# Kernel tuning notes

Hardware: AMD Instinct MI355X
Metric: run time of the kernel (lower is better)

## Reference

```python
import jax, jax.numpy as jnp
import numpy as np

B, T, HID = 2, 2048, 1024
H, DK, DV = 8, 128, 128      # num_heads, head_f_dim (key), head_i_dim (value)
LR = 128                     # gate low-rank dim
EPS = 1e-5


def setup_inputs() -> dict:
    key = jax.random.key(0)
    ks = jax.random.split(key, 8)
    def w(k, shape, fan_in):
        return jax.random.normal(k, shape, jnp.float32) / np.float32(np.sqrt(fan_in))
    return {
        "hidden_states": jax.random.normal(ks[0], (B, T, HID), jnp.float32),
        "Wq": w(ks[1], (HID, HID), HID),   # key_dim x hidden
        "Wk": w(ks[2], (HID, HID), HID),
        "Wv": w(ks[3], (HID, HID), HID),   # value_dim x hidden
        "Wg1": w(ks[4], (LR, HID), HID),   # low-rank gate down
        "Wg2": w(ks[5], (HID, LR), LR),    # low-rank gate up
        "g_norm_weight": jnp.ones((HID,), jnp.float32),
        "Wo": w(ks[6], (HID, HID), HID),
    }


def _lightnet_fwd(x, Wq, Wk, Wv, Wg1, Wg2, g_norm_weight, Wo):
    b, t, _ = x.shape
    q = jax.nn.silu(x @ Wq.T).reshape(b, t, H, DK)
    k = (x @ Wk.T).reshape(b, t, H, DK)
    v = (x @ Wv.T).reshape(b, t, H, DV)

    # LightNet gating: normalized keys via logcumsumexp over time
    z = jax.lax.cumlogsumexp(k, axis=1)                 # [b,t,h,dk]
    k = jnp.exp(k - z)                                  # exp-normalized keys
    g = jnp.concatenate([z[:, :1], z[:, :-1]], axis=1) - z  # <= 0; g[:,0]=0

    scale = DK ** -0.5

    # gated linear attention recurrence: S_t = exp(g_t) * S_{t-1} + k_t v_t^T
    def step(S, inp):
        qt, kt, vt, gt = inp                            # [b,h,dk],[b,h,dk],[b,h,dv],[b,h,dk]
        S = jnp.exp(gt)[..., None] * S + kt[..., None] * vt[..., None, :]
        o = jnp.einsum('bhk,bhkv->bhv', qt, S) * scale
        return S, o

    S0 = jnp.zeros((b, H, DK, DV), x.dtype)
    tfirst = lambda a: jnp.moveaxis(a, 1, 0)
    _, oT = jax.lax.scan(step, S0, (tfirst(q), tfirst(k), tfirst(v), tfirst(g)))
    o = jnp.moveaxis(oT, 0, 1).reshape(b, t, H * DV)    # [b,t,hidden]

    # RMSNorm(o) * swish(gate) then output projection
    gate = (x @ Wg1.T) @ Wg2.T
    o = o * jax.lax.rsqrt(jnp.mean(o * o, axis=-1, keepdims=True) + EPS) * g_norm_weight
    o = o * gate * jax.nn.sigmoid(gate)
    return o @ Wo.T


def reference(hidden_states, Wq, Wk, Wv, Wg1, Wg2, g_norm_weight, Wo):
    return _lightnet_fwd(hidden_states, Wq, Wk, Wv, Wg1, Wg2, g_norm_weight, Wo)
```

## Files before the change

kernel.cpp:

```cpp
#include <hip/hip_runtime.h>
#include <hip/hip_bf16.h>
#include <stdint.h>


typedef short short8 __attribute__((ext_vector_type(8)));
typedef float f32x4 __attribute__((ext_vector_type(4)));

#define T_SEQ 2048
#define HIDN  1024
#define SCALE 0.08838834764831845f
#define LDSP  136

__device__ __forceinline__ float blo(unsigned int u){
  union{unsigned int i; float f;} v; v.i = u << 16; return v.f;
}
__device__ __forceinline__ float bhi(unsigned int u){
  union{unsigned int i; float f;} v; v.i = u & 0xffff0000u; return v.f;
}
__device__ __forceinline__ float bu2f(unsigned short u){
  union{unsigned int i; float f;} v; v.i = ((unsigned int)u) << 16; return v.f;
}
__device__ __forceinline__ unsigned short f2bu(float f){
  union{float f; unsigned int i;} v; v.f = f;
  unsigned int x = v.i;
  x += 0x7fffu + ((x >> 16) & 1u);
  return (unsigned short)(x >> 16);
}
__device__ __forceinline__ void up8(const unsigned short* p, float* f){
  uint4 v = *(const uint4*)p;
  f[0]=blo(v.x); f[1]=bhi(v.x); f[2]=blo(v.y); f[3]=bhi(v.y);
  f[4]=blo(v.z); f[5]=bhi(v.z); f[6]=blo(v.w); f[7]=bhi(v.w);
}
__device__ __forceinline__ void async16(const void* g, void* l){
  __builtin_amdgcn_global_load_lds(
      (const __attribute__((address_space(1))) unsigned int*)g,
      (__attribute__((address_space(3))) unsigned int*)l, 16, 0, 0);
}

__global__ __launch_bounds__(256) void convert_all(
    const float* __restrict__ X,  const float* __restrict__ Wq,
    const float* __restrict__ Wk, const float* __restrict__ Wv,
    const float* __restrict__ Wg1,const float* __restrict__ Wg2,
    const float* __restrict__ gnw,const float* __restrict__ Wo,
    unsigned short* __restrict__ base, float* __restrict__ SumSq)
{
  int q = blockIdx.x * 256 + threadIdx.x;
  const float* src; unsigned short* dst; int rel = q;
  if (rel < 1048576)            { src = X;   dst = base;            }
  else if ((rel -= 1048576) < 262144) { src = Wq;  dst = base + 4194304; }
  else if ((rel -=  262144) < 262144) { src = Wk;  dst = base + 5242880; }
  else if ((rel -=  262144) < 262144) { src = Wv;  dst = base + 6291456; }
  else if ((rel -=  262144) < 262144) { src = Wo;  dst = base + 7340032; }
  else if ((rel -=  262144) <  32768) { src = Wg1; dst = base + 8388608; }
  else if ((rel -=   32768) <  32768) { src = Wg2; dst = base + 8519680; }
  else if ((rel -=   32768) <    256) { src = gnw; dst = base + 8650752; }
  else { rel -= 256;
    ((float4*)SumSq)[rel] = make_float4(0.f,0.f,0.f,0.f); return; }
  float4 v = ((const float4*)src)[rel];
  ushort4 o; o.x=f2bu(v.x); o.y=f2bu(v.y); o.z=f2bu(v.z); o.w=f2bu(v.w);
  ((ushort4*)dst)[rel] = o;
}

__device__ __forceinline__ void gemm_core(
    const unsigned short* __restrict__ A, const unsigned short* __restrict__ B,
    int K, int row0, int col0,
    unsigned short* sA, unsigned short* sB, f32x4 acc[4][4], int tid)
{
  const int lane = tid & 63;
  const int wm = (tid >> 6) & 1, wn = tid >> 7;
  const int wb = tid & 192;
  for (int k0 = 0; k0 < K; k0 += 64){
    __syncthreads();
#pragma unroll
    for (int h = 0; h < 2; ++h){
#pragma unroll
      for (int r = 0; r < 2; ++r){
        int idx  = r*256 + tid;
        int mrow = idx >> 2, kc = (idx & 3) * 8;
        async16(A + (size_t)(row0 + mrow)*K + k0 + h*32 + kc,
                sA + (size_t)(h*512 + r*256 + wb)*8);
        async16(B + (size_t)(col0 + mrow)*K + k0 + h*32 + kc,
                sB + (size_t)(h*512 + r*256 + wb)*8);
      }
    }
    __syncthreads();
#pragma unroll
    for (int h = 0; h < 2; ++h){
      short8 av[4], bv[4];
#pragma unroll
      for (int i=0;i<4;i++)
        av[i] = *(const short8*)(sA + h*4096 + (size_t)(wm*64 + i*16 + (lane&15))*32 + (lane>>4)*8);
#pragma unroll
      for (int j=0;j<4;j++)
        bv[j] = *(const short8*)(sB + h*4096 + (size_t)(wn*64 + j*16 + (lane&15))*32 + (lane>>4)*8);
#pragma unroll
      for (int i=0;i<4;i++)
#pragma unroll
        for (int j=0;j<4;j++)
          acc[i][j] = __builtin_amdgcn_mfma_f32_16x16x32_bf16(av[i], bv[j], acc[i][j], 0, 0, 0);
    }
  }
}

__device__ __forceinline__ void epilogue_lds(
    f32x4 acc[4][4], int row0, int col0, int tid, int ldc, int act,
    unsigned short* __restrict__ Cb, unsigned short* sC)
{
  const int lane = tid & 63;
  const int wm = (tid >> 6) & 1, wn = tid >> 7;
#pragma unroll
  for (int p=0;p<4;p++){
    __syncthreads();
    if (wm == (p>>1)){
#pragma unroll
      for (int ii=0; ii<2; ii++){
        int i = (p&1)*2 + ii;
        int lr = i*16 + ((lane>>4)<<2) - (p&1)*32;
#pragma unroll
        for (int j=0;j<4;j++){
          int col = wn*64 + j*16 + (lane&15);
#pragma unroll
          for (int r=0;r<4;r++){
            float v = acc[i][j][r];
            if (act == 1) v = v / (1.f + __expf(-v));
            else if (act == 2) v = __expf(v);
            sC[(lr+r)*128 + col] = f2bu(v);
          }
        }
      }
    }
    __syncthreads();
#pragma unroll
    for (int c = tid; c < 512; c += 256){
      int rr = c >> 4, off = (c & 15)*8;
      *(uint4*)&Cb[(size_t)(row0 + p*32 + rr)*ldc + col0 + off] =
          *(const uint4*)&sC[rr*128 + off];
    }
  }
}

__device__ __forceinline__ void epilogue_f32(
    f32x4 acc[4][4], int row0, int col0, int tid, int ldc,
    float* __restrict__ Cf)
{
  const int lane = tid & 63;
  const int wm = (tid >> 6) & 1, wn = tid >> 7;
#pragma unroll
  for (int i=0;i<4;i++){
    int rbase = row0 + wm*64 + i*16 + ((lane>>4)<<2);
#pragma unroll
    for (int j=0;j<4;j++){
      int col = col0 + wn*64 + j*16 + (lane&15);
#pragma unroll
      for (int r=0;r<4;r++)
        Cf[(size_t)(rbase + r)*ldc + col] = acc[i][j][r];
    }
  }
}

__global__ __launch_bounds__(256, 4) void proj_kernel(
    const unsigned short* __restrict__ X,
    const unsigned short* __restrict__ Wq, const unsigned short* __restrict__ Wk,
    const unsigned short* __restrict__ Wv, const unsigned short* __restrict__ Wg1,
    unsigned short* __restrict__ Qb, unsigned short* __restrict__ Eb,
    unsigned short* __restrict__ Vb, unsigned short* __restrict__ G1b)
{
  __shared__ unsigned short sA[128*64], sB[128*64];
  int tid = threadIdx.x;
  int which = blockIdx.y >> 3;
  const unsigned short* Bp = (which==0)?Wq:(which==1)?Wk:(which==2)?Wv:Wg1;
  int row0 = blockIdx.x * 128;
  int col0 = (which==3) ? 0 : (blockIdx.y & 7) * 128;
  f32x4 acc[4][4] = {};
  gemm_core(X, Bp, HIDN, row0, col0, sA, sB, acc, tid);
  if      (which==0) epilogue_lds(acc,row0,col0,tid,HIDN,1,Qb, sA);
  else if (which==1) epilogue_lds(acc,row0,col0,tid,HIDN,2,Eb, sA);
  else if (which==2) epilogue_lds(acc,row0,col0,tid,HIDN,0,Vb, sA);
  else               epilogue_lds(acc,row0,col0,tid,128 ,0,G1b,sA);
}

__global__ __launch_bounds__(256, 4) void gemm_bt(
    const unsigned short* __restrict__ A, const unsigned short* __restrict__ B,
    int K, int ldc, int act, float* __restrict__ Cf,
    unsigned short* __restrict__ Cb)
{
  __shared__ unsigned short sA[128*64], sB[128*64];
  int tid = threadIdx.x;
  int row0 = blockIdx.x * 128, col0 = blockIdx.y * 128;
  f32x4 acc[4][4] = {};
  gemm_core(A, B, K, row0, col0, sA, sB, acc, tid);
  if (Cb) epilogue_lds(acc, row0, col0, tid, ldc, act, Cb, sA);
  else    epilogue_f32(acc, row0, col0, tid, ldc, Cf);
}

__global__ __launch_bounds__(512, 2) void attn_pass1(
    const unsigned short* __restrict__ Eb, const unsigned short* __restrict__ Vb,
    unsigned short* __restrict__ U, float* __restrict__ Esum)
{
  __shared__ unsigned short Vt[128*LDSP], Et[128*LDSP];
  __shared__ float seg_part[4*128];
  int tid = threadIdx.x;
  const int lane = tid & 63, quad = lane >> 4;
  const int w = tid >> 6, wm = w & 3, wn = w >> 2;
  const int Rb = wm*32, Cb = wn*64;
  int bh = blockIdx.x >> 4, ch = blockIdx.x & 15;
  int b = bh >> 3, h = bh & 7;
  size_t rowbase = (size_t)(b*T_SEQ + ch*128)*HIDN + h*128;

#pragma unroll
  for (int i=0;i<4;i++){
    int u = tid + i*512; int t = u >> 4, kc = (u & 15)*8;
    unsigned short tmp[8];
    *(uint4*)tmp = *(const uint4*)&Vb[rowbase + (size_t)t*HIDN + kc];
#pragma unroll
    for (int j=0;j<8;j++) Vt[(kc+j)*LDSP + t] = tmp[j];
    *(uint4*)tmp = *(const uint4*)&Eb[rowbase + (size_t)t*HIDN + kc];
#pragma unroll
    for (int j=0;j<8;j++) Et[(kc+j)*LDSP + t] = tmp[j];
  }
  __syncthreads();

  {
    int seg = tid >> 7, k = tid & 127;
    float s = 0.f;
    for (int c = seg*32; c < seg*32+32; ++c) s += bu2f(Et[k*LDSP + c]);
    seg_part[seg*128 + k] = s;
  }
  __syncthreads();
  if (tid < 128)
    Esum[(size_t)blockIdx.x*128 + tid] =
        seg_part[tid] + seg_part[128+tid] + seg_part[256+tid] + seg_part[384+tid];

  f32x4 acc[2][4] = {};
  short8 av[2], bv[4];
#pragma unroll
  for (int s0=0; s0<128; s0+=32){
#pragma unroll
    for (int i=0;i<2;i++)
      av[i] = *(const short8*)(Vt + (Rb + i*16 + (lane&15))*LDSP + s0 + quad*8);
#pragma unroll
    for (int j=0;j<4;j++)
      bv[j] = *(const short8*)(Et + (Cb + j*16 + (lane&15))*LDSP + s0 + quad*8);
#pragma unroll
    for (int i=0;i<2;i++)
#pragma unroll
      for (int j=0;j<4;j++)
        acc[i][j] = __builtin_amdgcn_mfma_f32_16x16x32_bf16(av[i], bv[j], acc[i][j], 0,0,0);
  }
  __syncthreads();

#pragma unroll
  for (int i=0;i<2;i++)
#pragma unroll
    for (int j=0;j<4;j++){
      int k = Cb + j*16 + (lane&15);
#pragma unroll
      for (int r=0;r<4;r++){
        int v = Rb + i*16 + quad*4 + r;
        Et[v*LDSP + k] = f2bu(acc[i][j][r]);
      }
    }
  __syncthreads();
  unsigned short* Ub = U + (size_t)blockIdx.x*16384;
#pragma unroll
  for (int i=0;i<4;i++){
    int u = tid + i*512; int v = u >> 4, kc = (u & 15)*8;
    *(uint4*)&Ub[v*128 + kc] = *(const uint4*)&Et[v*LDSP + kc];
  }
}

__global__ __launch_bounds__(256) void attn_pass2(
    unsigned short* __restrict__ U, float* __restrict__ Esum)
{
  int bh = blockIdx.x >> 4, sl = blockIdx.x & 15;
  int p = sl*1024 + threadIdx.x*4;
  float r0=0.f, r1=0.f, r2=0.f, r3=0.f;
  for (int c=0;c<16;c++){
    ushort4* ptr = (ushort4*)&U[(size_t)(bh*16 + c)*16384 + p];
    ushort4 t = *ptr;
    ushort4 w;
    w.x=f2bu(r0); w.y=f2bu(r1); w.z=f2bu(r2); w.w=f2bu(r3);
    *ptr = w;
    r0 += bu2f(t.x); r1 += bu2f(t.y); r2 += bu2f(t.z); r3 += bu2f(t.w);
  }
  if (sl == 0 && threadIdx.x < 128){
    float r = 0.f;
    for (int c=0;c<16;c++){
      float* q = &Esum[(size_t)(bh*16 + c)*128 + threadIdx.x];
      float t = *q; *q = r; r += t;
    }
  }
}

__global__ __launch_bounds__(512, 4) void attn_pass3(
    const unsigned short* __restrict__ Eb, const unsigned short* __restrict__ Qb,
    const unsigned short* __restrict__ Vb, const unsigned short* __restrict__ U,
    const float* __restrict__ Esum, unsigned short* __restrict__ Oatt,
    float* __restrict__ SumSq)
{
  __shared__ unsigned short smem[2*128*LDSP];
  __shared__ float seg_part[4*128];
  unsigned short* bufA = smem;
  unsigned short* bufB = smem + 128*LDSP;

  int tid = threadIdx.x;
  const int lane = tid & 63, quad = lane >> 4;
  const int w = tid >> 6, wm = w & 3, wn = w >> 2;
  const int Rb = wm*32, Cb = wn*64;
  int bh = blockIdx.x >> 4, ch = blockIdx.x & 15;
  int b = bh >> 3, h = bh & 7;
  size_t rowbase = (size_t)(b*T_SEQ + ch*128)*HIDN + h*128;
  const unsigned short* Ublk = U + (size_t)blockIdx.x*16384;

#pragma unroll
  for (int i=0;i<4;i++){
    int u = tid + i*512; int t = u >> 4, kc = (u & 15)*8;
    *(uint4*)&bufA[t*LDSP + kc] = *(const uint4*)&Qb[rowbase + (size_t)t*HIDN + kc];
    *(uint4*)&bufB[t*LDSP + kc] = *(const uint4*)&Eb[rowbase + (size_t)t*HIDN + kc];
  }
  __syncthreads();

  {
    int col = tid & 127, seg = tid >> 7;
    float psum = 0.f;
    for (int s = seg*32; s < seg*32+32; ++s) psum += bu2f(bufB[s*LDSP + col]);
    seg_part[seg*128 + col] = psum;
    __syncthreads();
    float run = Esum[(size_t)blockIdx.x*128 + col];
    for (int ss=0; ss<4; ++ss) if (ss < seg) run += seg_part[ss*128 + col];
    for (int s = seg*32; s < seg*32+32; ++s){
      run += bu2f(bufB[s*LDSP + col]);
      float q = bu2f(bufA[s*LDSP + col]);
      bufA[s*LDSP + col] = f2bu(q * SCALE * __builtin_amdgcn_rcpf(run));
    }
  }
  __syncthreads();

  f32x4 accO[2][4] = {}, accP[2][4] = {};
  short8 av[2], bv[4];
#pragma unroll
  for (int k0=0; k0<128; k0+=32){
#pragma unroll
    for (int i=0;i<2;i++)
      av[i] = *(const short8*)(bufA + (Rb + i*16 + (lane&15))*LDSP + k0 + quad*8);
#pragma unroll
    for (int j=0;j<4;j++)
      bv[j] = *(const short8*)(Ublk + (size_t)(Cb + j*16 + (lane&15))*128 + k0 + quad*8);
#pragma unroll
    for (int i=0;i<2;i++)
#pragma unroll
      for (int j=0;j<4;j++)
        accO[i][j] = __builtin_amdgcn_mfma_f32_16x16x32_bf16(av[i], bv[j], accO[i][j], 0,0,0);
#pragma unroll
    for (int j=0;j<4;j++)
      bv[j] = *(const short8*)(bufB + (Cb + j*16 + (lane&15))*LDSP + k0 + quad*8);
#pragma unroll
    for (int i=0;i<2;i++)
#pragma unroll
      for (int j=0;j<4;j++)
        accP[i][j] = __builtin_amdgcn_mfma_f32_16x16x32_bf16(av[i], bv[j], accP[i][j], 0,0,0);
  }
  __syncthreads();

#pragma unroll
  for (int i=0;i<2;i++){
#pragma unroll
    for (int j=0;j<4;j++){
      int s = Cb + j*16 + (lane&15);
#pragma unroll
      for (int r=0;r<4;r++){
        int t = Rb + i*16 + quad*4 + r;
        bufA[t*LDSP + s] = f2bu(s <= t ? accP[i][j][r] : 0.f);
      }
    }
  }
#pragma unroll
  for (int i=0;i<4;i++){
    int u = tid + i*512; int t = u >> 4, kc = (u & 15)*8;
    unsigned short tmp[8];
    *(uint4*)tmp = *(const uint4*)&Vb[rowbase + (size_t)t*HIDN + kc];
#pragma unroll
    for (int j=0;j<8;j++) bufB[(kc+j)*LDSP + t] = tmp[j];
  }
  __syncthreads();

#pragma unroll
  for (int k0=0; k0<128; k0+=32){
#pragma unroll
    for (int i=0;i<2;i++)
      av[i] = *(const short8*)(bufA + (Rb + i*16 + (lane&15))*LDSP + k0 + quad*8);
#pragma unroll
    for (int j=0;j<4;j++)
      bv[j] = *(const short8*)(bufB + (Cb + j*16 + (lane&15))*LDSP + k0 + quad*8);
#pragma unroll
    for (int i=0;i<2;i++)
#pragma unroll
      for (int j=0;j<4;j++)
        accO[i][j] = __builtin_amdgcn_mfma_f32_16x16x32_bf16(av[i], bv[j], accO[i][j], 0,0,0);
  }
  __syncthreads();

#pragma unroll
  for (int i=0;i<2;i++){
#pragma unroll
    for (int j=0;j<4;j++){
      int v = Cb + j*16 + (lane&15);
#pragma unroll
      for (int r=0;r<4;r++){
        int t = Rb + i*16 + quad*4 + r;
        bufA[t*LDSP + v] = f2bu(accO[i][j][r]);
      }
    }
  }
  __syncthreads();

  {
    int seg = tid >> 7, row = tid & 127;
    float s = 0.f;
    for (int c = seg*32; c < seg*32+32; ++c){
      float x = bu2f(bufA[row*LDSP + c]); s += x*x;
    }
    seg_part[seg*128 + row] = s;
  }
#pragma unroll
  for (int i=0;i<4;i++){
    int u = tid + i*512; int t = u >> 4, kc = (u & 15)*8;
    *(uint4*)&Oatt[rowbase + (size_t)t*HIDN + kc] = *(const uint4*)&bufA[t*LDSP + kc];
  }
  __syncthreads();
  if (tid < 128){
    float s = seg_part[tid] + seg_part[128+tid] + seg_part[256+tid] + seg_part[384+tid];
    atomicAdd(&SumSq[(size_t)b*T_SEQ + ch*128 + tid], s);
  }
}

__global__ __launch_bounds__(256) void norm_gate2(
    const unsigned short* __restrict__ Oatt, const unsigned short* __restrict__ Gt,
    const unsigned short* __restrict__ gnw, const float* __restrict__ SumSq,
    unsigned short* __restrict__ Onorm)
{
  int row = blockIdx.x, tid = threadIdx.x;
  float rstd = rsqrtf(SumSq[row] * (1.f/1024.f) + 1e-5f);
  ushort4 o4 = *(const ushort4*)&Oatt[(size_t)row*HIDN + tid*4];
  ushort4 g4 = *(const ushort4*)&Gt  [(size_t)row*HIDN + tid*4];
  ushort4 w4 = *(const ushort4*)&gnw[tid*4];
  ushort4 r4;
  r4.x = f2bu(bu2f(o4.x) * rstd * bu2f(w4.x) * bu2f(g4.x));
  r4.y = f2bu(bu2f(o4.y) * rstd * bu2f(w4.y) * bu2f(g4.y));
  r4.z = f2bu(bu2f(o4.z) * rstd * bu2f(w4.z) * bu2f(g4.z));
  r4.w = f2bu(bu2f(o4.w) * rstd * bu2f(w4.w) * bu2f(g4.w));
  *(ushort4*)&Onorm[(size_t)row*HIDN + tid*4] = r4;
}

extern "C" void kernel_launch(void* const* d_in, const int* in_sizes, int n_in,
                              void* d_out, int out_size, void* d_ws, size_t ws_size,
                              hipStream_t stream) {
  unsigned short* wsS = (unsigned short*)d_ws;

  unsigned short* Xc   = wsS;
  unsigned short* Wqc  = wsS + 4194304;
  unsigned short* Wkc  = wsS + 5242880;
  unsigned short* Wvc  = wsS + 6291456;
  unsigned short* Woc  = wsS + 7340032;
  unsigned short* Wg1c = wsS + 8388608;
  unsigned short* Wg2c = wsS + 8519680;
  unsigned short* gnwc = wsS + 8650752;
  unsigned short* Qb   = wsS + 8651776;
  unsigned short* Eb   = wsS + 12846080;
  unsigned short* Vb   = wsS + 17040384;
  unsigned short* G1b  = wsS + 21234688;
  unsigned short* Gt   = wsS + 21758976;
  unsigned short* Ub   = wsS + 25953280;
  unsigned short* Oattb= wsS + 30147584;
  float*          Esum = (float*)(wsS + 34341888);
  float*          SumSq= (float*)(wsS + 34407424);
  unsigned short* Onorm = Qb;

  convert_all<<<8453, 256, 0, stream>>>(
      (const float*)d_in[0], (const float*)d_in[1], (const float*)d_in[2],
      (const float*)d_in[3], (const float*)d_in[4], (const float*)d_in[5],
      (const float*)d_in[6], (const float*)d_in[7], wsS, SumSq);

  proj_kernel<<<dim3(32,25), 256, 0, stream>>>(Xc, Wqc, Wkc, Wvc, Wg1c, Qb, Eb, Vb, G1b);
  gemm_bt   <<<dim3(32,8),  256, 0, stream>>>(G1b, Wg2c, 128, HIDN, 1, nullptr, Gt);
  attn_pass1<<<256, 512, 0, stream>>>(Eb, Vb, Ub, Esum);
  attn_pass2<<<256, 256, 0, stream>>>(Ub, Esum);
  attn_pass3<<<256, 512, 0, stream>>>(Eb, Qb, Vb, Ub, Esum, Oattb, SumSq);
  norm_gate2<<<4096, 256, 0, stream>>>(Oattb, Gt, gnwc, SumSq, Onorm);
  gemm_bt   <<<dim3(32,8),  256, 0, stream>>>(Onorm, Woc, HIDN, HIDN, 0,
                                              (float*)d_out, nullptr);
}
```

Measured before the change: 206.2 us.

## Fuse attention passes and norm-gate into one cooperative kernel with grid syncs

Merges the three chunked-attention passes and the RMSNorm/gate kernel into a single cooperative kernel, using grid-wide syncs between the phases. Each block keeps its attention output tile in LDS and applies the norm and gate directly from there. This removes three kernel launches and the intermediate Oatt write and read through global memory. In exchange it pays for three grid barriers and requires all 256 blocks to be co-resident, and launch bounds no longer hint occupancy.

```diff
diff --git a/kernel.cpp b/kernel.cpp
--- a/kernel.cpp
+++ b/kernel.cpp
@@ -1,6 +1,9 @@
 #include <hip/hip_runtime.h>
 #include <hip/hip_bf16.h>
+#include <hip/hip_cooperative_groups.h>
 #include <stdint.h>
+
+namespace cg = cooperative_groups;
 
 
 typedef short short8 __attribute__((ext_vector_type(8)));
@@ -193,17 +196,25 @@
   else    epilogue_f32(acc, row0, col0, tid, ldc, Cf);
 }
 
-__global__ __launch_bounds__(512, 2) void attn_pass1(
-    const unsigned short* __restrict__ Eb, const unsigned short* __restrict__ Vb,
-    unsigned short* __restrict__ U, float* __restrict__ Esum)
-{
-  __shared__ unsigned short Vt[128*LDSP], Et[128*LDSP];
+__global__ __launch_bounds__(512) void attn_fused(
+    const unsigned short* __restrict__ Eb, const unsigned short* __restrict__ Qb,
+    const unsigned short* __restrict__ Vb, unsigned short* __restrict__ U,
+    float* __restrict__ Esum, float* __restrict__ SumSq,
+    const unsigned short* __restrict__ Gt, const unsigned short* __restrict__ gnw,
+    unsigned short* __restrict__ Onorm)
+{
+  cg::grid_group gridg = cg::this_grid();
+  __shared__ unsigned short smem[2*128*LDSP];
   __shared__ float seg_part[4*128];
+  unsigned short* bufA = smem;
+  unsigned short* bufB = smem + 128*LDSP;
+
   int tid = threadIdx.x;
   const int lane = tid & 63, quad = lane >> 4;
   const int w = tid >> 6, wm = w & 3, wn = w >> 2;
-  const int Rb = wm*32, Cb = wn*64;
-  int bh = blockIdx.x >> 4, ch = blockIdx.x & 15;
+  const int Rb = wm*32, Cbnd = wn*64;
+  int blk = blockIdx.x;
+  int bh = blk >> 4, ch = blk & 15;
   int b = bh >> 3, h = bh & 7;
   size_t rowbase = (size_t)(b*T_SEQ + ch*128)*HIDN + h*128;
 
@@ -213,104 +224,88 @@
     unsigned short tmp[8];
     *(uint4*)tmp = *(const uint4*)&Vb[rowbase + (size_t)t*HIDN + kc];
 #pragma unroll
-    for (int j=0;j<8;j++) Vt[(kc+j)*LDSP + t] = tmp[j];
+    for (int j=0;j<8;j++) bufA[(kc+j)*LDSP + t] = tmp[j];
     *(uint4*)tmp = *(const uint4*)&Eb[rowbase + (size_t)t*HIDN + kc];
 #pragma unroll
-    for (int j=0;j<8;j++) Et[(kc+j)*LDSP + t] = tmp[j];
+    for (int j=0;j<8;j++) bufB[(kc+j)*LDSP + t] = tmp[j];
   }
   __syncthreads();
 
   {
     int seg = tid >> 7, k = tid & 127;
     float s = 0.f;
-    for (int c = seg*32; c < seg*32+32; ++c) s += bu2f(Et[k*LDSP + c]);
+    for (int c = seg*32; c < seg*32+32; ++c) s += bu2f(bufB[k*LDSP + c]);
     seg_part[seg*128 + k] = s;
   }
   __syncthreads();
   if (tid < 128)
-    Esum[(size_t)blockIdx.x*128 + tid] =
+    Esum[(size_t)blk*128 + tid] =
         seg_part[tid] + seg_part[128+tid] + seg_part[256+tid] + seg_part[384+tid];
 
-  f32x4 acc[2][4] = {};
-  short8 av[2], bv[4];
-#pragma unroll
-  for (int s0=0; s0<128; s0+=32){
+  {
+    f32x4 acc[2][4] = {};
+    short8 av[2], bv[4];
+#pragma unroll
+    for (int s0=0; s0<128; s0+=32){
+#pragma unroll
+      for (int i=0;i<2;i++)
+        av[i] = *(const short8*)(bufA + (Rb + i*16 + (lane&15))*LDSP + s0 + quad*8);
+#pragma unroll
+      for (int j=0;j<4;j++)
+        bv[j] = *(const short8*)(bufB + (Cbnd + j*16 + (lane&15))*LDSP + s0 + quad*8);
+#pragma unroll
+      for (int i=0;i<2;i++)
+#pragma unroll
+        for (int j=0;j<4;j++)
+          acc[i][j] = __builtin_amdgcn_mfma_f32_16x16x32_bf16(av[i], bv[j], acc[i][j], 0,0,0);
+    }
+    __syncthreads();
 #pragma unroll
     for (int i=0;i<2;i++)
-      av[i] = *(const short8*)(Vt + (Rb + i*16 + (lane&15))*LDSP + s0 + quad*8);
-#pragma unroll
-    for (int j=0;j<4;j++)
-      bv[j] = *(const short8*)(Et + (Cb + j*16 + (lane&15))*LDSP + s0 + quad*8);
-#pragma unroll
-    for (int i=0;i<2;i++)
-#pragma unroll
-      for (int j=0;j<4;j++)
-        acc[i][j] = __builtin_amdgcn_mfma_f32_16x16x32_bf16(av[i], bv[j], acc[i][j], 0,0,0);
-  }
-  __syncthreads();
-
-#pragma unroll
-  for (int i=0;i<2;i++)
-#pragma unroll
-    for (int j=0;j<4;j++){
-      int k = Cb + j*16 + (lane&15);
-#pragma unroll
-      for (int r=0;r<4;r++){
-        int v = Rb + i*16 + quad*4 + r;
-        Et[v*LDSP + k] = f2bu(acc[i][j][r]);
-      }
-    }
-  __syncthreads();
-  unsigned short* Ub = U + (size_t)blockIdx.x*16384;
-#pragma unroll
-  for (int i=0;i<4;i++){
-    int u = tid + i*512; int v = u >> 4, kc = (u & 15)*8;
-    *(uint4*)&Ub[v*128 + kc] = *(const uint4*)&Et[v*LDSP + kc];
-  }
-}
-
-__global__ __launch_bounds__(256) void attn_pass2(
-    unsigned short* __restrict__ U, float* __restrict__ Esum)
-{
-  int bh = blockIdx.x >> 4, sl = blockIdx.x & 15;
-  int p = sl*1024 + threadIdx.x*4;
-  float r0=0.f, r1=0.f, r2=0.f, r3=0.f;
-  for (int c=0;c<16;c++){
-    ushort4* ptr = (ushort4*)&U[(size_t)(bh*16 + c)*16384 + p];
-    ushort4 t = *ptr;
-    ushort4 w;
-    w.x=f2bu(r0); w.y=f2bu(r1); w.z=f2bu(r2); w.w=f2bu(r3);
-    *ptr = w;
-    r0 += bu2f(t.x); r1 += bu2f(t.y); r2 += bu2f(t.z); r3 += bu2f(t.w);
-  }
-  if (sl == 0 && threadIdx.x < 128){
-    float r = 0.f;
-    for (int c=0;c<16;c++){
-      float* q = &Esum[(size_t)(bh*16 + c)*128 + threadIdx.x];
-      float t = *q; *q = r; r += t;
-    }
-  }
-}
-
-__global__ __launch_bounds__(512, 4) void attn_pass3(
-    const unsigned short* __restrict__ Eb, const unsigned short* __restrict__ Qb,
-    const unsigned short* __restrict__ Vb, const unsigned short* __restrict__ U,
-    const float* __restrict__ Esum, unsigned short* __restrict__ Oatt,
-    float* __restrict__ SumSq)
-{
-  __shared__ unsigned short smem[2*128*LDSP];
-  __shared__ float seg_part[4*128];
-  unsigned short* bufA = smem;
-  unsigned short* bufB = smem + 128*LDSP;
-
-  int tid = threadIdx.x;
-  const int lane = tid & 63, quad = lane >> 4;
-  const int w = tid >> 6, wm = w & 3, wn = w >> 2;
-  const int Rb = wm*32, Cb = wn*64;
-  int bh = blockIdx.x >> 4, ch = blockIdx.x & 15;
-  int b = bh >> 3, h = bh & 7;
-  size_t rowbase = (size_t)(b*T_SEQ + ch*128)*HIDN + h*128;
-  const unsigned short* Ublk = U + (size_t)blockIdx.x*16384;
+#pragma unroll
+      for (int j=0;j<4;j++){
+        int k = Cbnd + j*16 + (lane&15);
+#pragma unroll
+        for (int r=0;r<4;r++){
+          int v = Rb + i*16 + quad*4 + r;
+          bufB[v*LDSP + k] = f2bu(acc[i][j][r]);
+        }
+      }
+    __syncthreads();
+    unsigned short* Ub = U + (size_t)blk*16384;
+#pragma unroll
+    for (int i=0;i<4;i++){
+      int u = tid + i*512; int v = u >> 4, kc = (u & 15)*8;
+      *(uint4*)&Ub[v*128 + kc] = *(const uint4*)&bufB[v*LDSP + kc];
+    }
+  }
+  __threadfence();
+  gridg.sync();
+
+  {
+    int sl = blk & 15;
+    if (tid < 256){
+      int p = sl*1024 + tid*4;
+      float r0=0.f, r1=0.f, r2=0.f, r3=0.f;
+      for (int c=0;c<16;c++){
+        ushort4* ptr = (ushort4*)&U[(size_t)(bh*16 + c)*16384 + p];
+        ushort4 t = *ptr;
+        ushort4 wv;
+        wv.x=f2bu(r0); wv.y=f2bu(r1); wv.z=f2bu(r2); wv.w=f2bu(r3);
+        *ptr = wv;
+        r0 += bu2f(t.x); r1 += bu2f(t.y); r2 += bu2f(t.z); r3 += bu2f(t.w);
+      }
+    }
+    if (sl == 0 && tid < 128){
+      float r = 0.f;
+      for (int c=0;c<16;c++){
+        float* q = &Esum[(size_t)(bh*16 + c)*128 + tid];
+        float t = *q; *q = r; r += t;
+      }
+    }
+  }
+  __threadfence();
+  gridg.sync();
 
 #pragma unroll
   for (int i=0;i<4;i++){
@@ -326,7 +321,7 @@
     for (int s = seg*32; s < seg*32+32; ++s) psum += bu2f(bufB[s*LDSP + col]);
     seg_part[seg*128 + col] = psum;
     __syncthreads();
-    float run = Esum[(size_t)blockIdx.x*128 + col];
+    float run = Esum[(size_t)blk*128 + col];
     for (int ss=0; ss<4; ++ss) if (ss < seg) run += seg_part[ss*128 + col];
     for (int s = seg*32; s < seg*32+32; ++s){
       run += bu2f(bufB[s*LDSP + col]);
@@ -337,28 +332,31 @@
   __syncthreads();
 
   f32x4 accO[2][4] = {}, accP[2][4] = {};
-  short8 av[2], bv[4];
-#pragma unroll
-  for (int k0=0; k0<128; k0+=32){
-#pragma unroll
-    for (int i=0;i<2;i++)
-      av[i] = *(const short8*)(bufA + (Rb + i*16 + (lane&15))*LDSP + k0 + quad*8);
-#pragma unroll
-    for (int j=0;j<4;j++)
-      bv[j] = *(const short8*)(Ublk + (size_t)(Cb + j*16 + (lane&15))*128 + k0 + quad*8);
-#pragma unroll
-    for (int i=0;i<2;i++)
+  {
+    const unsigned short* Ublk = U + (size_t)blk*16384;
+    short8 av[2], bv[4];
+#pragma unroll
+    for (int k0=0; k0<128; k0+=32){
+#pragma unroll
+      for (int i=0;i<2;i++)
+        av[i] = *(const short8*)(bufA + (Rb + i*16 + (lane&15))*LDSP + k0 + quad*8);
 #pragma unroll
       for (int j=0;j<4;j++)
-        accO[i][j] = __builtin_amdgcn_mfma_f32_16x16x32_bf16(av[i], bv[j], accO[i][j], 0,0,0);
-#pragma unroll
-    for (int j=0;j<4;j++)
-      bv[j] = *(const short8*)(bufB + (Cb + j*16 + (lane&15))*LDSP + k0 + quad*8);
-#pragma unroll
-    for (int i=0;i<2;i++)
+        bv[j] = *(const short8*)(Ublk + (size_t)(Cbnd + j*16 + (lane&15))*128 + k0 + quad*8);
+#pragma unroll
+      for (int i=0;i<2;i++)
+#pragma unroll
+        for (int j=0;j<4;j++)
+          accO[i][j] = __builtin_amdgcn_mfma_f32_16x16x32_bf16(av[i], bv[j], accO[i][j], 0,0,0);
 #pragma unroll
       for (int j=0;j<4;j++)
-        accP[i][j] = __builtin_amdgcn_mfma_f32_16x16x32_bf16(av[i], bv[j], accP[i][j], 0,0,0);
+        bv[j] = *(const short8*)(bufB + (Cbnd + j*16 + (lane&15))*LDSP + k0 + quad*8);
+#pragma unroll
+      for (int i=0;i<2;i++)
+#pragma unroll
+        for (int j=0;j<4;j++)
+          accP[i][j] = __builtin_amdgcn_mfma_f32_16x16x32_bf16(av[i], bv[j], accP[i][j], 0,0,0);
+    }
   }
   __syncthreads();
 
@@ -366,7 +364,7 @@
   for (int i=0;i<2;i++){
 #pragma unroll
     for (int j=0;j<4;j++){
-      int s = Cb + j*16 + (lane&15);
+      int s = Cbnd + j*16 + (lane&15);
 #pragma unroll
       for (int r=0;r<4;r++){
         int t = Rb + i*16 + quad*4 + r;
@@ -384,19 +382,22 @@
   }
   __syncthreads();
 
-#pragma unroll
-  for (int k0=0; k0<128; k0+=32){
-#pragma unroll
-    for (int i=0;i<2;i++)
-      av[i] = *(const short8*)(bufA + (Rb + i*16 + (lane&15))*LDSP + k0 + quad*8);
-#pragma unroll
-    for (int j=0;j<4;j++)
-      bv[j] = *(const short8*)(bufB + (Cb + j*16 + (lane&15))*LDSP + k0 + quad*8);
-#pragma unroll
-    for (int i=0;i<2;i++)
+  {
+    short8 av[2], bv[4];
+#pragma unroll
+    for (int k0=0; k0<128; k0+=32){
+#pragma unroll
+      for (int i=0;i<2;i++)
+        av[i] = *(const short8*)(bufA + (Rb + i*16 + (lane&15))*LDSP + k0 + quad*8);
 #pragma unroll
       for (int j=0;j<4;j++)
-        accO[i][j] = __builtin_amdgcn_mfma_f32_16x16x32_bf16(av[i], bv[j], accO[i][j], 0,0,0);
+        bv[j] = *(const short8*)(bufB + (Cbnd + j*16 + (lane&15))*LDSP + k0 + quad*8);
+#pragma unroll
+      for (int i=0;i<2;i++)
+#pragma unroll
+        for (int j=0;j<4;j++)
+          accO[i][j] = __builtin_amdgcn_mfma_f32_16x16x32_bf16(av[i], bv[j], accO[i][j], 0,0,0);
+    }
   }
   __syncthreads();
 
@@ -404,7 +405,7 @@
   for (int i=0;i<2;i++){
 #pragma unroll
     for (int j=0;j<4;j++){
-      int v = Cb + j*16 + (lane&15);
+      int v = Cbnd + j*16 + (lane&15);
 #pragma unroll
       for (int r=0;r<4;r++){
         int t = Rb + i*16 + quad*4 + r;
@@ -422,34 +423,27 @@
     }
     seg_part[seg*128 + row] = s;
   }
-#pragma unroll
-  for (int i=0;i<4;i++){
-    int u = tid + i*512; int t = u >> 4, kc = (u & 15)*8;
-    *(uint4*)&Oatt[rowbase + (size_t)t*HIDN + kc] = *(const uint4*)&bufA[t*LDSP + kc];
-  }
   __syncthreads();
   if (tid < 128){
     float s = seg_part[tid] + seg_part[128+tid] + seg_part[256+tid] + seg_part[384+tid];
     atomicAdd(&SumSq[(size_t)b*T_SEQ + ch*128 + tid], s);
   }
-}
-
-__global__ __launch_bounds__(256) void norm_gate2(
-    const unsigned short* __restrict__ Oatt, const unsigned short* __restrict__ Gt,
-    const unsigned short* __restrict__ gnw, const float* __restrict__ SumSq,
-    unsigned short* __restrict__ Onorm)
-{
-  int row = blockIdx.x, tid = threadIdx.x;
-  float rstd = rsqrtf(SumSq[row] * (1.f/1024.f) + 1e-5f);
-  ushort4 o4 = *(const ushort4*)&Oatt[(size_t)row*HIDN + tid*4];
-  ushort4 g4 = *(const ushort4*)&Gt  [(size_t)row*HIDN + tid*4];
-  ushort4 w4 = *(const ushort4*)&gnw[tid*4];
-  ushort4 r4;
-  r4.x = f2bu(bu2f(o4.x) * rstd * bu2f(w4.x) * bu2f(g4.x));
-  r4.y = f2bu(bu2f(o4.y) * rstd * bu2f(w4.y) * bu2f(g4.y));
-  r4.z = f2bu(bu2f(o4.z) * rstd * bu2f(w4.z) * bu2f(g4.z));
-  r4.w = f2bu(bu2f(o4.w) * rstd * bu2f(w4.w) * bu2f(g4.w));
-  *(ushort4*)&Onorm[(size_t)row*HIDN + tid*4] = r4;
+  __threadfence();
+  gridg.sync();
+
+#pragma unroll
+  for (int i=0;i<4;i++){
+    int u = tid + i*512; int t = u >> 4, kc = (u & 15)*8;
+    float rstd = rsqrtf(SumSq[(size_t)b*T_SEQ + ch*128 + t] * (1.f/1024.f) + 1e-5f);
+    float o[8], g[8], wv[8];
+    up8(&bufA[t*LDSP + kc], o);
+    up8(&Gt[rowbase + (size_t)t*HIDN + kc], g);
+    up8(&gnw[h*128 + kc], wv);
+    unsigned short r8[8];
+#pragma unroll
+    for (int j=0;j<8;j++) r8[j] = f2bu(o[j] * rstd * wv[j] * g[j]);
+    *(uint4*)&Onorm[rowbase + (size_t)t*HIDN + kc] = *(const uint4*)r8;
+  }
 }
 
 extern "C" void kernel_launch(void* const* d_in, const int* in_sizes, int n_in,
@@ -471,7 +465,6 @@
   unsigned short* G1b  = wsS + 21234688;
   unsigned short* Gt   = wsS + 21758976;
   unsigned short* Ub   = wsS + 25953280;
-  unsigned short* Oattb= wsS + 30147584;
   float*          Esum = (float*)(wsS + 34341888);
   float*          SumSq= (float*)(wsS + 34407424);
   unsigned short* Onorm = Qb;
@@ -483,10 +476,20 @@
 
   proj_kernel<<<dim3(32,25), 256, 0, stream>>>(Xc, Wqc, Wkc, Wvc, Wg1c, Qb, Eb, Vb, G1b);
   gemm_bt   <<<dim3(32,8),  256, 0, stream>>>(G1b, Wg2c, 128, HIDN, 1, nullptr, Gt);
-  attn_pass1<<<256, 512, 0, stream>>>(Eb, Vb, Ub, Esum);
-  attn_pass2<<<256, 256, 0, stream>>>(Ub, Esum);
-  attn_pass3<<<256, 512, 0, stream>>>(Eb, Qb, Vb, Ub, Esum, Oattb, SumSq);
-  norm_gate2<<<4096, 256, 0, stream>>>(Oattb, Gt, gnwc, SumSq, Onorm);
+
+  {
+    const unsigned short* aEb = Eb; const unsigned short* aQb = Qb;
+    const unsigned short* aVb = Vb; unsigned short* aUb = Ub;
+    float* aEsum = Esum; float* aSumSq = SumSq;
+    const unsigned short* aGt = Gt; const unsigned short* agnw = gnwc;
+    unsigned short* aOn = Onorm;
+    void* kargs[] = { (void*)&aEb, (void*)&aQb, (void*)&aVb, (void*)&aUb,
+                      (void*)&aEsum, (void*)&aSumSq, (void*)&aGt, (void*)&agnw,
+                      (void*)&aOn };
+    hipLaunchCooperativeKernel((void*)attn_fused, dim3(256), dim3(512),
+                               kargs, 0, stream);
+  }
+
   gemm_bt   <<<dim3(32,8),  256, 0, stream>>>(Onorm, Woc, HIDN, HIDN, 0,
                                               (float*)d_out, nullptr);
 }
```

After: 433.6 us. 2.1x slower.
